# Performance work log

Hardware: AMD Instinct MI355X
Metric: run time of the kernel (lower is better)

## Reference

```python
import jax, jax.numpy as jnp
import numpy as np
from jax import lax

TAU_MEM = 100.0   # 1/0.01 default
V_LEAK = 0.0
V_TH = 1.0


def setup_inputs() -> dict:
    key = jax.random.key(0)
    k1, k2 = jax.random.split(key)
    B, T, F = 32, 128, 2048
    inp = jax.random.normal(k1, (B, T, F), dtype=jnp.float32)
    W = jax.random.normal(k2, (F, F), dtype=jnp.float32) * (1.0 / np.sqrt(F))
    b = jnp.zeros((F,), dtype=jnp.float32)
    return {"input": inp, "W": W, "b": b}


def _heaviside(x):
    return (x > 0).astype(x.dtype)


def reference(input, W, b):
    # time-distributed kernel: Linear applied to all timesteps at once
    gs = jnp.einsum('btn,mn->btm', input, W) + b  # [B, T, F]
    dt_over_tau = 1.0 / TAU_MEM

    def step(v, g):
        # Euler LIF update with delta (subtractive) reset
        v_new = v + dt_over_tau * ((V_LEAK - v) + g)
        z = _heaviside(v_new - V_TH)
        v_reset = v_new - z * V_TH
        return v_reset, z

    v0 = jnp.zeros(gs.shape[::2], dtype=gs.dtype)  # [B, F]
    _, zs = lax.scan(step, v0, jnp.moveaxis(gs, 1, 0))  # zs: [T, B, F]
    return jnp.moveaxis(zs, 0, 1)  # [B, T, F]
```

## Files before the change

kernel.cpp:

```cpp
#include <hip/hip_runtime.h>
#include <hip/hip_bf16.h>
#include <stdint.h>

#define Bdim 32
#define Tdim 128
#define Fdim 2048
#define Mdim (Bdim*Tdim)

#define BM 128
#define BN 128
#define BK 32

typedef __attribute__((ext_vector_type(8))) short bf16x8;
typedef __attribute__((ext_vector_type(4))) float f32x4;

__device__ inline unsigned short f2bf(float f) {
    union { float f; unsigned u; } x; x.f = f;
    unsigned r = (x.u + 0x7fffu + ((x.u >> 16) & 1u)) >> 16;
    return (unsigned short)r;
}

__global__ void convert_kernel(const float* __restrict__ A, const float* __restrict__ W,
                               unsigned short* __restrict__ a16, unsigned short* __restrict__ w16) {
    const int nA4 = (Mdim * Fdim) / 4;
    const int nW4 = (Fdim * Fdim) / 4;
    const int stride = gridDim.x * blockDim.x;
    for (int i = blockIdx.x * blockDim.x + threadIdx.x; i < nA4 + nW4; i += stride) {
        const float4* src; unsigned short* dst; int j;
        if (i < nA4) { src = (const float4*)A; dst = a16; j = i; }
        else         { src = (const float4*)W; dst = w16; j = i - nA4; }
        float4 v = src[j];
        ushort4 o;
        o.x = f2bf(v.x); o.y = f2bf(v.y); o.z = f2bf(v.z); o.w = f2bf(v.w);
        *(ushort4*)(dst + 4 * (size_t)j) = o;
    }
}

__global__ __launch_bounds__(256) void gemm_kernel(const unsigned short* __restrict__ A,
                                                   const unsigned short* __restrict__ Wm,
                                                   float* __restrict__ C) {
    __shared__ __align__(16) unsigned short sA[BM * BK];
    __shared__ __align__(16) unsigned short sB[BN * BK];

    const int tid = threadIdx.x;
    const int wid = tid >> 6, lane = tid & 63;
    const int wr = wid >> 1, wc = wid & 1;
    const int m0 = blockIdx.y * BM, n0 = blockIdx.x * BN;

    f32x4 acc[4][4];
#pragma unroll
    for (int i = 0; i < 4; i++)
#pragma unroll
        for (int j = 0; j < 4; j++) acc[i][j] = f32x4{0.f, 0.f, 0.f, 0.f};

    const int off0 = wid * 2048 + lane * 16;
    const int frow = lane & 15, fk = (lane >> 4) * 8;

    for (int kt = 0; kt < Fdim / BK; ++kt) {
        const int k0 = kt * BK;
#pragma unroll
        for (int j = 0; j < 2; ++j) {
            const int off  = off0 + j * 1024;
            const int row  = off >> 6;
            const int cole = (off & 63) >> 1;
            const unsigned short* ga = A  + (size_t)(m0 + row) * Fdim + k0 + cole;
            const unsigned short* gb = Wm + (size_t)(n0 + row) * Fdim + k0 + cole;
            __builtin_amdgcn_global_load_lds(
                (const __attribute__((address_space(1))) void*)ga,
                (__attribute__((address_space(3))) void*)(sA + (wid * 2048 + j * 1024) / 2),
                16, 0, 0);
            __builtin_amdgcn_global_load_lds(
                (const __attribute__((address_space(1))) void*)gb,
                (__attribute__((address_space(3))) void*)(sB + (wid * 2048 + j * 1024) / 2),
                16, 0, 0);
        }
        __syncthreads();

        bf16x8 af[4], bfr[4];
#pragma unroll
        for (int mi = 0; mi < 4; mi++)
            af[mi] = *(const bf16x8*)(sA + (wr * 64 + mi * 16 + frow) * BK + fk);
#pragma unroll
        for (int ni = 0; ni < 4; ni++)
            bfr[ni] = *(const bf16x8*)(sB + (wc * 64 + ni * 16 + frow) * BK + fk);
#pragma unroll
        for (int mi = 0; mi < 4; mi++)
#pragma unroll
            for (int ni = 0; ni < 4; ni++)
                acc[mi][ni] = __builtin_amdgcn_mfma_f32_16x16x32_bf16(af[mi], bfr[ni], acc[mi][ni], 0, 0, 0);
        __syncthreads();
    }

    const int crow = m0 + wr * 64 + (lane >> 4) * 4;
    const int ccol = n0 + wc * 64 + (lane & 15);
#pragma unroll
    for (int mi = 0; mi < 4; mi++)
#pragma unroll
        for (int ni = 0; ni < 4; ni++) {
            float* cp = C + (size_t)(crow + mi * 16) * Fdim + ccol + ni * 16;
#pragma unroll
            for (int r = 0; r < 4; r++) cp[(size_t)r * Fdim] = acc[mi][ni][r];
        }
}

__global__ void gemm_f32_naive(const float* __restrict__ A, const float* __restrict__ W,
                               float* __restrict__ C) {
    int col = blockIdx.x * blockDim.x + threadIdx.x;
    int row = blockIdx.y;
    float s = 0.f;
    for (int k = 0; k < Fdim; k++) s += A[(size_t)row * Fdim + k] * W[(size_t)col * Fdim + k];
    C[(size_t)row * Fdim + col] = s;
}

__global__ void lif_kernel(float* __restrict__ gs, const float* __restrict__ bias) {
    int idx = blockIdx.x * blockDim.x + threadIdx.x;
    int b = idx >> 11, f = idx & (Fdim - 1);
    const float bf = bias[f];
    float* p = gs + (size_t)b * Tdim * Fdim + f;
    float v = 0.f;
#pragma unroll
    for (int t0 = 0; t0 < Tdim; t0 += 8) {
        float g[8];
#pragma unroll
        for (int j = 0; j < 8; j++) g[j] = p[(size_t)(t0 + j) * Fdim];
#pragma unroll
        for (int j = 0; j < 8; j++) {
            float vn = v + 0.01f * ((0.0f - v) + (g[j] + bf));
            float z = (vn > 1.0f) ? 1.0f : 0.0f;
            v = vn - z;
            p[(size_t)(t0 + j) * Fdim] = z;
        }
    }
}

extern "C" void kernel_launch(void* const* d_in, const int* in_sizes, int n_in,
                              void* d_out, int out_size, void* d_ws, size_t ws_size,
                              hipStream_t stream) {
    const float* inp  = (const float*)d_in[0];
    const float* W    = (const float*)d_in[1];
    const float* bias = (const float*)d_in[2];
    float* out = (float*)d_out;

    const size_t needA = (size_t)Mdim * Fdim * 2;
    const size_t needW = (size_t)Fdim * Fdim * 2;

    if (ws_size >= needA + needW) {
        unsigned short* a16 = (unsigned short*)d_ws;
        unsigned short* w16 = (unsigned short*)((char*)d_ws + needA);
        convert_kernel<<<2048, 256, 0, stream>>>(inp, W, a16, w16);
        dim3 grid(Fdim / BN, Mdim / BM);
        gemm_kernel<<<grid, 256, 0, stream>>>(a16, w16, out);
    } else {
        dim3 grid(Fdim / 256, Mdim);
        gemm_f32_naive<<<grid, 256, 0, stream>>>(inp, W, out);
    }
    lif_kernel<<<(Bdim * Fdim) / 256, 256, 0, stream>>>(out, bias);
}
```

Before: 163.9 us.

## Double-buffer GEMM LDS tiles with BK=64 and preload all LIF timesteps

```diff
diff --git a/kernel.cpp b/kernel.cpp
--- a/kernel.cpp
+++ b/kernel.cpp
@@ -9,7 +9,7 @@
 
 #define BM 128
 #define BN 128
-#define BK 32
+#define BK 64
 
 typedef __attribute__((ext_vector_type(8))) short bf16x8;
 typedef __attribute__((ext_vector_type(4))) float f32x4;
@@ -39,8 +39,8 @@
 __global__ __launch_bounds__(256) void gemm_kernel(const unsigned short* __restrict__ A,
                                                    const unsigned short* __restrict__ Wm,
                                                    float* __restrict__ C) {
-    __shared__ __align__(16) unsigned short sA[BM * BK];
-    __shared__ __align__(16) unsigned short sB[BN * BK];
+    __shared__ __align__(16) unsigned short sA[2][BM * BK];
+    __shared__ __align__(16) unsigned short sB[2][BN * BK];
 
     const int tid = threadIdx.x;
     const int wid = tid >> 6, lane = tid & 63;
@@ -53,42 +53,57 @@
 #pragma unroll
         for (int j = 0; j < 4; j++) acc[i][j] = f32x4{0.f, 0.f, 0.f, 0.f};
 
-    const int off0 = wid * 2048 + lane * 16;
     const int frow = lane & 15, fk = (lane >> 4) * 8;
 
-    for (int kt = 0; kt < Fdim / BK; ++kt) {
+    auto stage = [&](int buf, int kt) {
         const int k0 = kt * BK;
 #pragma unroll
-        for (int j = 0; j < 2; ++j) {
-            const int off  = off0 + j * 1024;
-            const int row  = off >> 6;
-            const int cole = (off & 63) >> 1;
+        for (int j = 0; j < 4; ++j) {
+            const int base = wid * 1024 + j * 4096;
+            const int off  = base + lane * 16;
+            const int row  = off >> 7;
+            const int cole = (off & 127) >> 1;
             const unsigned short* ga = A  + (size_t)(m0 + row) * Fdim + k0 + cole;
             const unsigned short* gb = Wm + (size_t)(n0 + row) * Fdim + k0 + cole;
             __builtin_amdgcn_global_load_lds(
                 (const __attribute__((address_space(1))) void*)ga,
-                (__attribute__((address_space(3))) void*)(sA + (wid * 2048 + j * 1024) / 2),
+                (__attribute__((address_space(3))) void*)((char*)&sA[buf][0] + base),
                 16, 0, 0);
             __builtin_amdgcn_global_load_lds(
                 (const __attribute__((address_space(1))) void*)gb,
-                (__attribute__((address_space(3))) void*)(sB + (wid * 2048 + j * 1024) / 2),
+                (__attribute__((address_space(3))) void*)((char*)&sB[buf][0] + base),
                 16, 0, 0);
         }
-        __syncthreads();
+    };
 
-        bf16x8 af[4], bfr[4];
+    stage(0, 0);
+    __syncthreads();
+
+    int cur = 0;
+    const int NT = Fdim / BK;
+    for (int kt = 0; kt < NT; ++kt) {
+        if (kt + 1 < NT) stage(cur ^ 1, kt + 1);
+
+        bf16x8 af[2][4], bfr[2][4];
 #pragma unroll
-        for (int mi = 0; mi < 4; mi++)
-            af[mi] = *(const bf16x8*)(sA + (wr * 64 + mi * 16 + frow) * BK + fk);
+        for (int kk = 0; kk < 2; kk++) {
 #pragma unroll
-        for (int ni = 0; ni < 4; ni++)
-            bfr[ni] = *(const bf16x8*)(sB + (wc * 64 + ni * 16 + frow) * BK + fk);
-#pragma unroll
-        for (int mi = 0; mi < 4; mi++)
+            for (int mi = 0; mi < 4; mi++)
+                af[kk][mi] = *(const bf16x8*)(&sA[cur][0] + (wr * 64 + mi * 16 + frow) * BK + kk * 32 + fk);
 #pragma unroll
             for (int ni = 0; ni < 4; ni++)
-                acc[mi][ni] = __builtin_amdgcn_mfma_f32_16x16x32_bf16(af[mi], bfr[ni], acc[mi][ni], 0, 0, 0);
+                bfr[kk][ni] = *(const bf16x8*)(&sB[cur][0] + (wc * 64 + ni * 16 + frow) * BK + kk * 32 + fk);
+        }
+#pragma unroll
+        for (int kk = 0; kk < 2; kk++)
+#pragma unroll
+            for (int mi = 0; mi < 4; mi++)
+#pragma unroll
+                for (int ni = 0; ni < 4; ni++)
+                    acc[mi][ni] = __builtin_amdgcn_mfma_f32_16x16x32_bf16(af[kk][mi], bfr[kk][ni], acc[mi][ni], 0, 0, 0);
+
         __syncthreads();
+        cur ^= 1;
     }
 
     const int crow = m0 + wr * 64 + (lane >> 4) * 4;
@@ -112,24 +127,24 @@
     C[(size_t)row * Fdim + col] = s;
 }
 
-__global__ void lif_kernel(float* __restrict__ gs, const float* __restrict__ bias) {
+__global__ __launch_bounds__(256, 1) void lif_kernel(float* __restrict__ gs,
+                                                     const float* __restrict__ bias) {
     int idx = blockIdx.x * blockDim.x + threadIdx.x;
     int b = idx >> 11, f = idx & (Fdim - 1);
     const float bf = bias[f];
     float* p = gs + (size_t)b * Tdim * Fdim + f;
+
+    float g[Tdim];
+#pragma unroll
+    for (int t = 0; t < Tdim; t++) g[t] = p[(size_t)t * Fdim];
+
     float v = 0.f;
 #pragma unroll
-    for (int t0 = 0; t0 < Tdim; t0 += 8) {
-        float g[8];
-#pragma unroll
-        for (int j = 0; j < 8; j++) g[j] = p[(size_t)(t0 + j) * Fdim];
-#pragma unroll
-        for (int j = 0; j < 8; j++) {
-            float vn = v + 0.01f * ((0.0f - v) + (g[j] + bf));
-            float z = (vn > 1.0f) ? 1.0f : 0.0f;
-            v = vn - z;
-            p[(size_t)(t0 + j) * Fdim] = z;
-        }
+    for (int t = 0; t < Tdim; t++) {
+        float vn = v + 0.01f * ((0.0f - v) + (g[t] + bf));
+        float z = (vn > 1.0f) ? 1.0f : 0.0f;
+        v = vn - z;
+        p[(size_t)t * Fdim] = z;
     }
 }
 
```

Result: slower. 177.8 us (+8.5%).
